# Kernel tuning notes

Measured on AMD Instinct MI355X. Metric: run time of the kernel, lower is better.

The kernel has to match this reference:

```python
import jax, jax.numpy as jnp
import numpy as np

SHAPES = [(64, 64), (32, 32), (16, 16), (8, 8)]  # (H, W) per level, sum HW = 5440
DIMS, NH, NLVL, NPTS, D_HEIGHT, NCAM, NQ, BS = 256, 8, 4, 8, 4, 6, 10000, 1


def ms_deform_attn(value, shapes, loc, attw):
    # value [B, sumHW, nH, dh]; loc [B, nq, nH, L, P, 2] in [0,1]; attw [B, nq, nH, L, P]
    B, _, nH, dh = value.shape
    nq, P = loc.shape[1], loc.shape[4]
    out = jnp.zeros((B, nH, nq, dh), value.dtype)
    start = 0
    for lvl, (h, w) in enumerate(shapes):
        v = value[:, start:start + h * w].transpose(0, 2, 1, 3)  # [B,nH,hw,dh]
        start += h * w
        l = loc[:, :, :, lvl].transpose(0, 2, 1, 3, 4)  # [B,nH,nq,P,2]
        x = l[..., 0] * w - 0.5
        y = l[..., 1] * h - 0.5
        x0, y0 = jnp.floor(x), jnp.floor(y)
        acc = jnp.zeros((B, nH, nq, P, dh), value.dtype)
        for dy in (0.0, 1.0):
            for dx in (0.0, 1.0):
                cx, cy = x0 + dx, y0 + dy
                wgt = (1.0 - jnp.abs(x - cx)) * (1.0 - jnp.abs(y - cy))
                valid = (cx >= 0) & (cx < w) & (cy >= 0) & (cy < h)
                xi = jnp.clip(cx, 0, w - 1).astype(jnp.int32)
                yi = jnp.clip(cy, 0, h - 1).astype(jnp.int32)
                idx = (yi * w + xi).reshape(B, nH, -1)  # [B,nH,nq*P]
                g = jnp.take_along_axis(v, idx[..., None], axis=2).reshape(B, nH, nq, P, dh)
                acc = acc + jnp.where(valid, wgt, 0.0)[..., None] * g
        aw = attw[:, :, :, lvl].transpose(0, 2, 1, 3)  # [B,nH,nq,P]
        out = out + jnp.einsum('bhqp,bhqpd->bhqd', aw, acc)
    return out.transpose(0, 2, 1, 3).reshape(B, nq, nH * dh)


def setup_inputs() -> dict:
    key = jax.random.key(0)
    ks = jax.random.split(key, 16)
    l = sum(h * w for h, w in SHAPES)
    s = 1.0 / np.sqrt(DIMS)
    inp = {
        'query': jax.random.normal(ks[0], (BS, NQ, DIMS), jnp.float32),
        'key': jax.random.normal(ks[1], (NCAM, l, BS, DIMS), jnp.float32),
        'value': jax.random.normal(ks[2], (NCAM, l, BS, DIMS), jnp.float32),
        'ref_points': jax.random.uniform(ks[3], (NCAM, BS, NQ, D_HEIGHT, 2), jnp.float32),
        'vox_mask': jax.random.randint(ks[4], (NCAM, BS, NQ, D_HEIGHT), 0, 2) > 0,
        'spatial_shapes': np.array(SHAPES, dtype=np.int64),
        'level_start_index': np.array([0, 4096, 5120, 5376], dtype=np.int64),
        'value_W': jax.random.uniform(ks[5], (DIMS, DIMS), jnp.float32, -s, s),
        'value_b': jnp.zeros((DIMS,), jnp.float32),
        'off_W': jax.random.normal(ks[6], (DIMS, NH * NLVL * NPTS * 2), jnp.float32) * 0.01,
        'off_b': jax.random.normal(ks[7], (NH * NLVL * NPTS * 2,), jnp.float32) * 0.1,
        'attw_W': jax.random.normal(ks[8], (DIMS, NH * NLVL * NPTS), jnp.float32) * 0.02,
        'attw_b': jnp.zeros((NH * NLVL * NPTS,), jnp.float32),
        'out_W': jax.random.uniform(ks[9], (DIMS, DIMS), jnp.float32, -s, s),
        'out_b': jnp.zeros((DIMS,), jnp.float32),
    }
    return inp


def reference(query, key, value, ref_points, vox_mask, spatial_shapes, level_start_index,
              value_W, value_b, off_W, off_b, attw_W, attw_b, out_W, out_b):
    shapes = [(int(h), int(w)) for h, w in np.asarray(spatial_shapes)]
    bs, nq, dims = query.shape
    cam = vox_mask.shape[0]
    B = bs * cam
    nH = NH
    dh = dims // nH
    Lv, P, D = len(shapes), NPTS, ref_points.shape[3]

    # value_proj; key unused by deformable attention math
    v = value.transpose(2, 0, 1, 3).reshape(B, -1, dims)
    v = (v @ value_W + value_b).reshape(B, -1, nH, dh)

    # rebatch: every camera sees the full (batch-0 visible) query set; padded
    # entries in the original are discarded, so computing all and masking is exact.
    q = jnp.broadcast_to(query[:, None], (bs, cam, nq, dims)).reshape(B, nq, dims)

    off = (q @ off_W + off_b).reshape(B, nq, nH, Lv, P, 2)
    attw = jax.nn.softmax((q @ attw_W + attw_b).reshape(B, nq, nH, Lv * P), -1)
    attw = attw.reshape(B, nq, nH, Lv, P)

    norm = jnp.array([[w, h] for h, w in shapes], q.dtype)  # [Lv,2] -> (W,H)
    off = off / norm[None, None, None, :, None, :]

    ref_rb = ref_points.transpose(1, 0, 2, 3, 4).reshape(B, nq, D, 2)
    off = off.reshape(B, nq, nH, Lv, P // D, D, 2)
    loc = (ref_rb[:, :, None, None, None] + off).reshape(B, nq, nH, Lv, P, 2)

    out = ms_deform_attn(v, shapes, loc, attw).reshape(bs, cam, nq, dims)

    valid = (vox_mask[:, 0].sum(-1) > 0).astype(q.dtype)  # [cam,nq] (batch-0 indexes, as original)
    slots = jnp.einsum('cq,bcqd->bqd', valid, out)
    count = (vox_mask.sum(-1) > 0).transpose(1, 2, 0).sum(-1).astype(q.dtype)
    count = jnp.maximum(count, 1.0)
    slots = slots / count[..., None]
    slots = slots @ out_W + out_b
    return slots + query  # dropout = identity (eval); inp_residual = query
```

## Files before the change

kernel.cpp:

```cpp
#include <hip/hip_runtime.h>


typedef unsigned short ushort_t;
typedef unsigned int uint_t;
typedef __attribute__((ext_vector_type(8))) short bf16x8;
typedef __attribute__((ext_vector_type(4))) float f32x4;
typedef __attribute__((ext_vector_type(2))) float f32x2;

__device__ __forceinline__ float bf2f(ushort_t u) {
    return __uint_as_float(((uint_t)u) << 16);
}
__device__ __forceinline__ ushort_t f2bf(float f) {
    uint_t i = __float_as_uint(f);
    uint_t r = i + 0x7fffu + ((i >> 16) & 1u);
    return (ushort_t)(r >> 16);
}
__device__ __forceinline__ bf16x8 pack8(float4 v0, float4 v1) {
    return (bf16x8){
        (short)f2bf(v0.x), (short)f2bf(v0.y), (short)f2bf(v0.z), (short)f2bf(v0.w),
        (short)f2bf(v1.x), (short)f2bf(v1.y), (short)f2bf(v1.z), (short)f2bf(v1.w)};
}

__global__ __launch_bounds__(256) void prep_w(
    const float* __restrict__ Wv, const float* __restrict__ Wo,
    const float* __restrict__ Wf, const float* __restrict__ Wa,
    ushort_t* __restrict__ Tv, ushort_t* __restrict__ To,
    ushort_t* __restrict__ Tqk) {
    const int z = blockIdx.z;
    const float* W;
    ushort_t* T;
    int N;
    if (z == 0)      { W = Wv; T = Tv;              N = 256; }
    else if (z == 1) { W = Wo; T = To;              N = 256; }
    else if (z == 2) { W = Wf; T = Tqk;             N = 512; }
    else             { W = Wa; T = Tqk + 512 * 256; N = 256; }
    const int n0 = blockIdx.y * 32;
    if (n0 >= N) return;
    const int k0 = blockIdx.x * 32;

    __shared__ float tile[32][33];
    const int tx = threadIdx.x & 31;
    const int ty = threadIdx.x >> 5;
    #pragma unroll
    for (int r = 0; r < 4; ++r) {
        const int k = ty + r * 8;
        tile[k][tx] = W[(size_t)(k0 + k) * N + n0 + tx];
    }
    __syncthreads();
    #pragma unroll
    for (int r = 0; r < 4; ++r) {
        const int n = ty + r * 8;
        T[(size_t)(n0 + n) * 256 + k0 + tx] = f2bf(tile[tx][n]);
    }
}

template <bool AF32, bool OUT_BF16, bool RESID>
__device__ __forceinline__ void gemm_body(
    ushort_t (*sA)[128][32], ushort_t (*sB)[128][32],
    const void* __restrict__ Av, const ushort_t* __restrict__ Wt,
    const float* __restrict__ bias0, const float* __restrict__ bias1, int split,
    const float* __restrict__ resid, void* __restrict__ Cv,
    int M, int N, int bx, int by) {
    const int m0 = bx * 128;
    const int n0 = by * 128;
    const int t    = threadIdx.x;
    const int lane = t & 63;
    const int w    = t >> 6;
    const int wr   = w >> 1, wc = w & 1;

    const int srow = t >> 2;
    const int skof = (t & 3) * 8;

    const bool am0 = (m0 + srow) < M;
    const bool am1 = (m0 + 64 + srow) < M;
    const float*    Af0 = (const float*)Av + (size_t)(m0 + srow) * 256 + skof;
    const float*    Af1 = Af0 + (size_t)64 * 256;
    const ushort_t* Ab0 = (const ushort_t*)Av + (size_t)(m0 + srow) * 256 + skof;
    const ushort_t* Ab1 = Ab0 + (size_t)64 * 256;
    const ushort_t* Bp0 = Wt + (size_t)(n0 + srow) * 256 + skof;
    const ushort_t* Bp1 = Bp0 + (size_t)64 * 256;

    const bf16x8 zz = {0, 0, 0, 0, 0, 0, 0, 0};

    auto loadA = [&](const float* af, const ushort_t* ab, int ko, bool ok) -> bf16x8 {
        if (!ok) return zz;
        if (AF32) {
            const float4 v0 = *(const float4*)(af + ko);
            const float4 v1 = *(const float4*)(af + ko + 4);
            return pack8(v0, v1);
        }
        return *(const bf16x8*)(ab + ko);
    };

    f32x4 acc[4][4];
    #pragma unroll
    for (int i = 0; i < 4; ++i)
        #pragma unroll
        for (int j = 0; j < 4; ++j)
            acc[i][j] = (f32x4){0.f, 0.f, 0.f, 0.f};

    {
        const bf16x8 a0 = loadA(Af0, Ab0, 0, am0);
        const bf16x8 a1 = loadA(Af1, Ab1, 0, am1);
        const bf16x8 b0 = *(const bf16x8*)(Bp0);
        const bf16x8 b1 = *(const bf16x8*)(Bp1);
        *(bf16x8*)(&sA[0][srow][skof])      = a0;
        *(bf16x8*)(&sA[0][64 + srow][skof]) = a1;
        *(bf16x8*)(&sB[0][srow][skof])      = b0;
        *(bf16x8*)(&sB[0][64 + srow][skof]) = b1;
    }
    __syncthreads();

    const int rl = lane & 15;
    const int kq = (lane >> 4) * 8;

    for (int k = 0; k < 8; ++k) {
        const int buf = k & 1;

        bf16x8 na0 = zz, na1 = zz, nb0 = zz, nb1 = zz;
        if (k < 7) {
            const int ko = (k + 1) * 32;
            na0 = loadA(Af0, Ab0, ko, am0);
            na1 = loadA(Af1, Ab1, ko, am1);
            nb0 = *(const bf16x8*)(Bp0 + ko);
            nb1 = *(const bf16x8*)(Bp1 + ko);
        }

        bf16x8 af[4], bfr[4];
        #pragma unroll
        for (int i = 0; i < 4; ++i)
            af[i] = *(const bf16x8*)(&sA[buf][wr * 64 + i * 16 + rl][kq]);
        #pragma unroll
        for (int j = 0; j < 4; ++j)
            bfr[j] = *(const bf16x8*)(&sB[buf][wc * 64 + j * 16 + rl][kq]);
        #pragma unroll
        for (int i = 0; i < 4; ++i)
            #pragma unroll
            for (int j = 0; j < 4; ++j)
                acc[i][j] = __builtin_amdgcn_mfma_f32_16x16x32_bf16(
                    af[i], bfr[j], acc[i][j], 0, 0, 0);

        if (k < 7) {
            __syncthreads();
            *(bf16x8*)(&sA[buf ^ 1][srow][skof])      = na0;
            *(bf16x8*)(&sA[buf ^ 1][64 + srow][skof]) = na1;
            *(bf16x8*)(&sB[buf ^ 1][srow][skof])      = nb0;
            *(bf16x8*)(&sB[buf ^ 1][64 + srow][skof]) = nb1;
            __syncthreads();
        }
    }

    const int col_l = lane & 15;
    const int rq    = (lane >> 4) * 4;
    #pragma unroll
    for (int j = 0; j < 4; ++j) {
        const int gn = n0 + wc * 64 + j * 16 + col_l;
        const float bj = (gn < split) ? bias0[gn] : bias1[gn - split];
        #pragma unroll
        for (int i = 0; i < 4; ++i) {
            #pragma unroll
            for (int r = 0; r < 4; ++r) {
                const int gm = m0 + wr * 64 + i * 16 + rq + r;
                if (gm >= M) continue;
                float v = acc[i][j][r] + bj;
                if (RESID) v += resid[(size_t)gm * N + gn];
                if (OUT_BF16)
                    ((ushort_t*)Cv)[(size_t)gm * N + gn] = f2bf(v);
                else
                    ((float*)Cv)[(size_t)gm * N + gn] = v;
            }
        }
    }
}

__global__ __launch_bounds__(256) void gemm_vqk(
    const float* __restrict__ value, const ushort_t* __restrict__ value_Wt,
    const float* __restrict__ value_b, ushort_t* __restrict__ vproj,
    const float* __restrict__ query, const ushort_t* __restrict__ qk_Wt,
    const float* __restrict__ off_b, const float* __restrict__ attw_b,
    float* __restrict__ qkcat) {
    __shared__ ushort_t sA[2][128][32];
    __shared__ ushort_t sB[2][128][32];
    int b = blockIdx.x;
    if (b < 510) {
        gemm_body<true, true, false>(sA, sB, value, value_Wt, value_b, value_b,
                                     256, nullptr, (void*)vproj, 32640, 256,
                                     b % 255, b / 255);
    } else {
        b -= 510;
        gemm_body<true, false, false>(sA, sB, query, qk_Wt, off_b, attw_b,
                                      512, nullptr, (void*)qkcat, 10000, 768,
                                      b % 79, b / 79);
    }
}

__global__ __launch_bounds__(256) void gemm_out_k(
    const ushort_t* __restrict__ slots, const ushort_t* __restrict__ out_Wt,
    const float* __restrict__ out_b, const float* __restrict__ query,
    float* __restrict__ out) {
    __shared__ ushort_t sA[2][128][32];
    __shared__ ushort_t sB[2][128][32];
    gemm_body<false, false, true>(sA, sB, slots, out_Wt, out_b, out_b, 256,
                                  query, (void*)out, 10000, 256,
                                  blockIdx.x, blockIdx.y);
}

__global__ __launch_bounds__(256) void sample_k(
    const float* __restrict__ qkcat,
    const float* __restrict__ refp,
    const int* __restrict__ vox,
    const ushort_t* __restrict__ vproj,
    ushort_t* __restrict__ slots) {
    const int q   = blockIdx.x;
    const int tid = threadIdx.x;
    const int lane  = tid & 63;
    const int h     = tid >> 5;
    const int lp    = tid & 31;
    const int slice = (tid >> 2) & 7;
    const int g     = tid & 3;

    __shared__ float s_valid[8];
    __shared__ float s_red[256][8];

    if (tid < 6) {
        const int base = (tid * 10000 + q) * 4;
        const int mm = vox[base] | vox[base + 1] | vox[base + 2] | vox[base + 3];
        s_valid[tid] = mm ? 1.0f : 0.0f;
    }

    const float a = qkcat[(size_t)q * 768 + 512 + tid];
    float mx = a;
    #pragma unroll
    for (int o = 16; o >= 1; o >>= 1) mx = fmaxf(mx, __shfl_xor(mx, o));
    const float e = __expf(a - mx);
    float se = e;
    #pragma unroll
    for (int o = 16; o >= 1; o >>= 1) se += __shfl_xor(se, o);
    const float aw = e / se;

    const int lvl = lp >> 3;
    const int p   = lp & 7;
    const int dd  = p & 3;
    const int   Sarr[4]   = {64, 32, 16, 8};
    const int   Lstart[4] = {0, 4096, 5120, 5376};
    const int   S  = Sarr[lvl];
    const float Sf = (float)S;
    const int   lstart = Lstart[lvl];
    const float ox = qkcat[(size_t)q * 768 + h * 64 + lvl * 16 + p * 2 + 0] / Sf;
    const float oy = qkcat[(size_t)q * 768 + h * 64 + lvl * 16 + p * 2 + 1] / Sf;

    __syncthreads();
    const float cnt = s_valid[0] + s_valid[1] + s_valid[2] +
                      s_valid[3] + s_valid[4] + s_valid[5];

    f32x2 acc2[4] = {{0.f, 0.f}, {0.f, 0.f}, {0.f, 0.f}, {0.f, 0.f}};
    const ushort_t* vp = vproj + (g << 3);
    const int srcbase = (lane & 32) + slice * 4;

    for (int c = 0; c < 6; ++c) {
        if (s_valid[c] == 0.0f) continue;

        int   ci0, ci1, ci2, ci3;
        float cw0, cw1, cw2, cw3;
        {
            const int rbase = ((c * 10000 + q) * 4 + dd) * 2;
            const float rx = refp[rbase + 0];
            const float ry = refp[rbase + 1];
            const float x  = (rx + ox) * Sf - 0.5f;
            const float y  = (ry + oy) * Sf - 0.5f;
            const float x0 = floorf(x), y0 = floorf(y);
            int   ci[4];
            float cw[4];
            #pragma unroll
            for (int k = 0; k < 4; ++k) {
                const float cx = x0 + (float)(k & 1);
                const float cy = y0 + (float)(k >> 1);
                const float wgt = (1.0f - fabsf(x - cx)) * (1.0f - fabsf(y - cy));
                const bool ok = (cx >= 0.0f) & (cx < Sf) & (cy >= 0.0f) & (cy < Sf);
                const int xi = (int)fminf(fmaxf(cx, 0.0f), Sf - 1.0f);
                const int yi = (int)fminf(fmaxf(cy, 0.0f), Sf - 1.0f);
                ci[k] = (c * 5440 + lstart + yi * S + xi) * 256 + h * 32;
                cw[k] = ok ? wgt * aw : 0.0f;
            }
            ci0 = ci[0]; ci1 = ci[1]; ci2 = ci[2]; ci3 = ci[3];
            cw0 = cw[0]; cw1 = cw[1]; cw2 = cw[2]; cw3 = cw[3];
        }

        #pragma unroll
        for (int j = 0; j < 4; ++j) {
            const int src = srcbase + j;
            const int i0 = __shfl(ci0, src), i1 = __shfl(ci1, src);
            const int i2 = __shfl(ci2, src), i3 = __shfl(ci3, src);
            const uint4 v0 = *(const uint4*)(vp + i0);
            const uint4 v1 = *(const uint4*)(vp + i1);
            const uint4 v2 = *(const uint4*)(vp + i2);
            const uint4 v3 = *(const uint4*)(vp + i3);
            const float w0 = __shfl(cw0, src), w1 = __shfl(cw1, src);
            const float w2 = __shfl(cw2, src), w3 = __shfl(cw3, src);
            const f32x2 W0 = {w0, w0}, W1 = {w1, w1}, W2 = {w2, w2}, W3 = {w3, w3};
            acc2[0] += W0 * (f32x2){__uint_as_float(v0.x << 16), __uint_as_float(v0.x & 0xffff0000u)};
            acc2[1] += W0 * (f32x2){__uint_as_float(v0.y << 16), __uint_as_float(v0.y & 0xffff0000u)};
            acc2[2] += W0 * (f32x2){__uint_as_float(v0.z << 16), __uint_as_float(v0.z & 0xffff0000u)};
            acc2[3] += W0 * (f32x2){__uint_as_float(v0.w << 16), __uint_as_float(v0.w & 0xffff0000u)};
            acc2[0] += W1 * (f32x2){__uint_as_float(v1.x << 16), __uint_as_float(v1.x & 0xffff0000u)};
            acc2[1] += W1 * (f32x2){__uint_as_float(v1.y << 16), __uint_as_float(v1.y & 0xffff0000u)};
            acc2[2] += W1 * (f32x2){__uint_as_float(v1.z << 16), __uint_as_float(v1.z & 0xffff0000u)};
            acc2[3] += W1 * (f32x2){__uint_as_float(v1.w << 16), __uint_as_float(v1.w & 0xffff0000u)};
            acc2[0] += W2 * (f32x2){__uint_as_float(v2.x << 16), __uint_as_float(v2.x & 0xffff0000u)};
            acc2[1] += W2 * (f32x2){__uint_as_float(v2.y << 16), __uint_as_float(v2.y & 0xffff0000u)};
            acc2[2] += W2 * (f32x2){__uint_as_float(v2.z << 16), __uint_as_float(v2.z & 0xffff0000u)};
            acc2[3] += W2 * (f32x2){__uint_as_float(v2.w << 16), __uint_as_float(v2.w & 0xffff0000u)};
            acc2[0] += W3 * (f32x2){__uint_as_float(v3.x << 16), __uint_as_float(v3.x & 0xffff0000u)};
            acc2[1] += W3 * (f32x2){__uint_as_float(v3.y << 16), __uint_as_float(v3.y & 0xffff0000u)};
            acc2[2] += W3 * (f32x2){__uint_as_float(v3.z << 16), __uint_as_float(v3.z & 0xffff0000u)};
            acc2[3] += W3 * (f32x2){__uint_as_float(v3.w << 16), __uint_as_float(v3.w & 0xffff0000u)};
        }
    }

    #pragma unroll
    for (int n = 0; n < 4; ++n) {
        s_red[tid][2 * n]     = acc2[n].x;
        s_red[tid][2 * n + 1] = acc2[n].y;
    }
    __syncthreads();

    const int cch = tid & 31;
    float sum = 0.0f;
    #pragma unroll
    for (int s = 0; s < 8; ++s)
        sum += s_red[h * 32 + s * 4 + (cch >> 3)][cch & 7];

    slots[(size_t)q * 256 + tid] = f2bf(sum / fmaxf(cnt, 1.0f));
}

extern "C" void kernel_launch(void* const* d_in, const int* in_sizes, int n_in,
                              void* d_out, int out_size, void* d_ws, size_t ws_size,
                              hipStream_t stream) {
    const float* query   = (const float*)d_in[0];
    const float* value   = (const float*)d_in[2];
    const float* refp    = (const float*)d_in[3];
    const int*   vox     = (const int*)d_in[4];
    const float* value_W = (const float*)d_in[7];
    const float* value_b = (const float*)d_in[8];
    const float* off_W   = (const float*)d_in[9];
    const float* off_b   = (const float*)d_in[10];
    const float* attw_W  = (const float*)d_in[11];
    const float* attw_b  = (const float*)d_in[12];
    const float* out_W   = (const float*)d_in[13];
    const float* out_b   = (const float*)d_in[14];
    float* out = (float*)d_out;

    char* ws = (char*)d_ws;
    ushort_t* vproj    = (ushort_t*)ws;
    float*    qkcat    = (float*)   (ws + 16711680);
    ushort_t* slots    = (ushort_t*)(ws + 47431680);
    ushort_t* value_Wt = (ushort_t*)(ws + 52551680);
    ushort_t* out_Wt   = (ushort_t*)(ws + 52551680 + 131072);
    ushort_t* qk_Wt    = (ushort_t*)(ws + 52551680 + 262144);

    prep_w<<<dim3(8, 16, 4), 256, 0, stream>>>(
        value_W, out_W, off_W, attw_W, value_Wt, out_Wt, qk_Wt);
    gemm_vqk<<<984, 256, 0, stream>>>(value, value_Wt, value_b, vproj,
                                      query, qk_Wt, off_b, attw_b, qkcat);
    sample_k<<<10000, 256, 0, stream>>>(qkcat, refp, vox, vproj, slots);
    gemm_out_k<<<dim3(79, 2), 256, 0, stream>>>(slots, out_Wt, out_b, query, out);
}
```

Baseline: 336.8 us.

## Store projected values in fp32, qk logits in bf16, reuse qkcat buffer for slots

Switches the value projection output to fp32 and the offset/attention-weight GEMM output to bf16, and writes the sampled slots back into the attention-logit region of the qkcat buffer, read with a 768 stride by the output GEMM. The bf16 packing is replaced with the hardware packed convert instruction via inline asm. The gather in the sampling kernel now loads twice the bytes per sampled value but avoids bf16 unpacking, while offsets and logits lose precision by going through bf16.

New measurement: 507.8 us. 50.8% more time.

```diff
diff --git a/kernel.cpp b/kernel.cpp
--- a/kernel.cpp
+++ b/kernel.cpp
@@ -16,9 +16,12 @@
     return (ushort_t)(r >> 16);
 }
 __device__ __forceinline__ bf16x8 pack8(float4 v0, float4 v1) {
-    return (bf16x8){
-        (short)f2bf(v0.x), (short)f2bf(v0.y), (short)f2bf(v0.z), (short)f2bf(v0.w),
-        (short)f2bf(v1.x), (short)f2bf(v1.y), (short)f2bf(v1.z), (short)f2bf(v1.w)};
+    union { uint_t u[4]; bf16x8 v; } r;
+    asm("v_cvt_pk_bf16_f32 %0, %1, %2" : "=v"(r.u[0]) : "v"(v0.x), "v"(v0.y));
+    asm("v_cvt_pk_bf16_f32 %0, %1, %2" : "=v"(r.u[1]) : "v"(v0.z), "v"(v0.w));
+    asm("v_cvt_pk_bf16_f32 %0, %1, %2" : "=v"(r.u[2]) : "v"(v1.x), "v"(v1.y));
+    asm("v_cvt_pk_bf16_f32 %0, %1, %2" : "=v"(r.u[3]) : "v"(v1.z), "v"(v1.w));
+    return r.v;
 }
 
 __global__ __launch_bounds__(256) void prep_w(
@@ -57,7 +60,7 @@
 template <bool AF32, bool OUT_BF16, bool RESID>
 __device__ __forceinline__ void gemm_body(
     ushort_t (*sA)[128][32], ushort_t (*sB)[128][32],
-    const void* __restrict__ Av, const ushort_t* __restrict__ Wt,
+    const void* __restrict__ Av, int Astride, const ushort_t* __restrict__ Wt,
     const float* __restrict__ bias0, const float* __restrict__ bias1, int split,
     const float* __restrict__ resid, void* __restrict__ Cv,
     int M, int N, int bx, int by) {
@@ -73,10 +76,10 @@
 
     const bool am0 = (m0 + srow) < M;
     const bool am1 = (m0 + 64 + srow) < M;
-    const float*    Af0 = (const float*)Av + (size_t)(m0 + srow) * 256 + skof;
-    const float*    Af1 = Af0 + (size_t)64 * 256;
-    const ushort_t* Ab0 = (const ushort_t*)Av + (size_t)(m0 + srow) * 256 + skof;
-    const ushort_t* Ab1 = Ab0 + (size_t)64 * 256;
+    const float*    Af0 = (const float*)Av + (size_t)(m0 + srow) * Astride + skof;
+    const float*    Af1 = Af0 + (size_t)64 * Astride;
+    const ushort_t* Ab0 = (const ushort_t*)Av + (size_t)(m0 + srow) * Astride + skof;
+    const ushort_t* Ab1 = Ab0 + (size_t)64 * Astride;
     const ushort_t* Bp0 = Wt + (size_t)(n0 + srow) * 256 + skof;
     const ushort_t* Bp1 = Bp0 + (size_t)64 * 256;
 
@@ -175,42 +178,42 @@
 
 __global__ __launch_bounds__(256) void gemm_vqk(
     const float* __restrict__ value, const ushort_t* __restrict__ value_Wt,
-    const float* __restrict__ value_b, ushort_t* __restrict__ vproj,
+    const float* __restrict__ value_b, float* __restrict__ vproj,
     const float* __restrict__ query, const ushort_t* __restrict__ qk_Wt,
     const float* __restrict__ off_b, const float* __restrict__ attw_b,
-    float* __restrict__ qkcat) {
+    ushort_t* __restrict__ qkcat) {
     __shared__ ushort_t sA[2][128][32];
     __shared__ ushort_t sB[2][128][32];
     int b = blockIdx.x;
     if (b < 510) {
-        gemm_body<true, true, false>(sA, sB, value, value_Wt, value_b, value_b,
-                                     256, nullptr, (void*)vproj, 32640, 256,
-                                     b % 255, b / 255);
+        gemm_body<true, false, false>(sA, sB, value, 256, value_Wt, value_b,
+                                      value_b, 256, nullptr, (void*)vproj,
+                                      32640, 256, b % 255, b / 255);
     } else {
         b -= 510;
-        gemm_body<true, false, false>(sA, sB, query, qk_Wt, off_b, attw_b,
-                                      512, nullptr, (void*)qkcat, 10000, 768,
-                                      b % 79, b / 79);
+        gemm_body<true, true, false>(sA, sB, query, 256, qk_Wt, off_b, attw_b,
+                                     512, nullptr, (void*)qkcat, 10000, 768,
+                                     b % 79, b / 79);
     }
 }
 
 __global__ __launch_bounds__(256) void gemm_out_k(
-    const ushort_t* __restrict__ slots, const ushort_t* __restrict__ out_Wt,
+    const ushort_t* __restrict__ slots,
+    const ushort_t* __restrict__ out_Wt,
     const float* __restrict__ out_b, const float* __restrict__ query,
     float* __restrict__ out) {
     __shared__ ushort_t sA[2][128][32];
     __shared__ ushort_t sB[2][128][32];
-    gemm_body<false, false, true>(sA, sB, slots, out_Wt, out_b, out_b, 256,
+    gemm_body<false, false, true>(sA, sB, slots, 768, out_Wt, out_b, out_b, 256,
                                   query, (void*)out, 10000, 256,
                                   blockIdx.x, blockIdx.y);
 }
 
 __global__ __launch_bounds__(256) void sample_k(
-    const float* __restrict__ qkcat,
+    ushort_t* __restrict__ qkcat,
     const float* __restrict__ refp,
     const int* __restrict__ vox,
-    const ushort_t* __restrict__ vproj,
-    ushort_t* __restrict__ slots) {
+    const float* __restrict__ vproj) {
     const int q   = blockIdx.x;
     const int tid = threadIdx.x;
     const int lane  = tid & 63;
@@ -228,7 +231,7 @@
         s_valid[tid] = mm ? 1.0f : 0.0f;
     }
 
-    const float a = qkcat[(size_t)q * 768 + 512 + tid];
+    const float a = bf2f(qkcat[(size_t)q * 768 + 512 + tid]);
     float mx = a;
     #pragma unroll
     for (int o = 16; o >= 1; o >>= 1) mx = fmaxf(mx, __shfl_xor(mx, o));
@@ -246,15 +249,15 @@
     const int   S  = Sarr[lvl];
     const float Sf = (float)S;
     const int   lstart = Lstart[lvl];
-    const float ox = qkcat[(size_t)q * 768 + h * 64 + lvl * 16 + p * 2 + 0] / Sf;
-    const float oy = qkcat[(size_t)q * 768 + h * 64 + lvl * 16 + p * 2 + 1] / Sf;
+    const float ox = bf2f(qkcat[(size_t)q * 768 + h * 64 + lvl * 16 + p * 2 + 0]) / Sf;
+    const float oy = bf2f(qkcat[(size_t)q * 768 + h * 64 + lvl * 16 + p * 2 + 1]) / Sf;
 
     __syncthreads();
     const float cnt = s_valid[0] + s_valid[1] + s_valid[2] +
                       s_valid[3] + s_valid[4] + s_valid[5];
 
     f32x2 acc2[4] = {{0.f, 0.f}, {0.f, 0.f}, {0.f, 0.f}, {0.f, 0.f}};
-    const ushort_t* vp = vproj + (g << 3);
+    const float* vp = vproj + (g << 3);
     const int srcbase = (lane & 32) + slice * 4;
 
     for (int c = 0; c < 6; ++c) {
@@ -291,29 +294,33 @@
             const int src = srcbase + j;
             const int i0 = __shfl(ci0, src), i1 = __shfl(ci1, src);
             const int i2 = __shfl(ci2, src), i3 = __shfl(ci3, src);
-            const uint4 v0 = *(const uint4*)(vp + i0);
-            const uint4 v1 = *(const uint4*)(vp + i1);
-            const uint4 v2 = *(const uint4*)(vp + i2);
-            const uint4 v3 = *(const uint4*)(vp + i3);
             const float w0 = __shfl(cw0, src), w1 = __shfl(cw1, src);
             const float w2 = __shfl(cw2, src), w3 = __shfl(cw3, src);
+            const f32x4 a0 = *(const f32x4*)(vp + i0);
+            const f32x4 b0 = *(const f32x4*)(vp + i0 + 4);
+            const f32x4 a1 = *(const f32x4*)(vp + i1);
+            const f32x4 b1 = *(const f32x4*)(vp + i1 + 4);
+            const f32x4 a2 = *(const f32x4*)(vp + i2);
+            const f32x4 b2 = *(const f32x4*)(vp + i2 + 4);
+            const f32x4 a3 = *(const f32x4*)(vp + i3);
+            const f32x4 b3 = *(const f32x4*)(vp + i3 + 4);
             const f32x2 W0 = {w0, w0}, W1 = {w1, w1}, W2 = {w2, w2}, W3 = {w3, w3};
-            acc2[0] += W0 * (f32x2){__uint_as_float(v0.x << 16), __uint_as_float(v0.x & 0xffff0000u)};
-            acc2[1] += W0 * (f32x2){__uint_as_float(v0.y << 16), __uint_as_float(v0.y & 0xffff0000u)};
-            acc2[2] += W0 * (f32x2){__uint_as_float(v0.z << 16), __uint_as_float(v0.z & 0xffff0000u)};
-            acc2[3] += W0 * (f32x2){__uint_as_float(v0.w << 16), __uint_as_float(v0.w & 0xffff0000u)};
-            acc2[0] += W1 * (f32x2){__uint_as_float(v1.x << 16), __uint_as_float(v1.x & 0xffff0000u)};
-            acc2[1] += W1 * (f32x2){__uint_as_float(v1.y << 16), __uint_as_float(v1.y & 0xffff0000u)};
-            acc2[2] += W1 * (f32x2){__uint_as_float(v1.z << 16), __uint_as_float(v1.z & 0xffff0000u)};
-            acc2[3] += W1 * (f32x2){__uint_as_float(v1.w << 16), __uint_as_float(v1.w & 0xffff0000u)};
-            acc2[0] += W2 * (f32x2){__uint_as_float(v2.x << 16), __uint_as_float(v2.x & 0xffff0000u)};
-            acc2[1] += W2 * (f32x2){__uint_as_float(v2.y << 16), __uint_as_float(v2.y & 0xffff0000u)};
-            acc2[2] += W2 * (f32x2){__uint_as_float(v2.z << 16), __uint_as_float(v2.z & 0xffff0000u)};
-            acc2[3] += W2 * (f32x2){__uint_as_float(v2.w << 16), __uint_as_float(v2.w & 0xffff0000u)};
-            acc2[0] += W3 * (f32x2){__uint_as_float(v3.x << 16), __uint_as_float(v3.x & 0xffff0000u)};
-            acc2[1] += W3 * (f32x2){__uint_as_float(v3.y << 16), __uint_as_float(v3.y & 0xffff0000u)};
-            acc2[2] += W3 * (f32x2){__uint_as_float(v3.z << 16), __uint_as_float(v3.z & 0xffff0000u)};
-            acc2[3] += W3 * (f32x2){__uint_as_float(v3.w << 16), __uint_as_float(v3.w & 0xffff0000u)};
+            acc2[0] += W0 * (f32x2){a0[0], a0[1]};
+            acc2[1] += W0 * (f32x2){a0[2], a0[3]};
+            acc2[2] += W0 * (f32x2){b0[0], b0[1]};
+            acc2[3] += W0 * (f32x2){b0[2], b0[3]};
+            acc2[0] += W1 * (f32x2){a1[0], a1[1]};
+            acc2[1] += W1 * (f32x2){a1[2], a1[3]};
+            acc2[2] += W1 * (f32x2){b1[0], b1[1]};
+            acc2[3] += W1 * (f32x2){b1[2], b1[3]};
+            acc2[0] += W2 * (f32x2){a2[0], a2[1]};
+            acc2[1] += W2 * (f32x2){a2[2], a2[3]};
+            acc2[2] += W2 * (f32x2){b2[0], b2[1]};
+            acc2[3] += W2 * (f32x2){b2[2], b2[3]};
+            acc2[0] += W3 * (f32x2){a3[0], a3[1]};
+            acc2[1] += W3 * (f32x2){a3[2], a3[3]};
+            acc2[2] += W3 * (f32x2){b3[0], b3[1]};
+            acc2[3] += W3 * (f32x2){b3[2], b3[3]};
         }
     }
 
@@ -330,7 +337,7 @@
     for (int s = 0; s < 8; ++s)
         sum += s_red[h * 32 + s * 4 + (cch >> 3)][cch & 7];
 
-    slots[(size_t)q * 256 + tid] = f2bf(sum / fmaxf(cnt, 1.0f));
+    qkcat[(size_t)q * 768 + 512 + tid] = f2bf(sum / fmaxf(cnt, 1.0f));
 }
 
 extern "C" void kernel_launch(void* const* d_in, const int* in_sizes, int n_in,
@@ -351,17 +358,17 @@
     float* out = (float*)d_out;
 
     char* ws = (char*)d_ws;
-    ushort_t* vproj    = (ushort_t*)ws;
-    float*    qkcat    = (float*)   (ws + 16711680);
-    ushort_t* slots    = (ushort_t*)(ws + 47431680);
-    ushort_t* value_Wt = (ushort_t*)(ws + 52551680);
-    ushort_t* out_Wt   = (ushort_t*)(ws + 52551680 + 131072);
-    ushort_t* qk_Wt    = (ushort_t*)(ws + 52551680 + 262144);
+    float*    vproj    = (float*)ws;
+    ushort_t* qkcat    = (ushort_t*)(ws + 33423360);
+    ushort_t* value_Wt = (ushort_t*)(ws + 48783360);
+    ushort_t* out_Wt   = (ushort_t*)(ws + 48783360 + 131072);
+    ushort_t* qk_Wt    = (ushort_t*)(ws + 48783360 + 262144);
 
     prep_w<<<dim3(8, 16, 4), 256, 0, stream>>>(
         value_W, out_W, off_W, attw_W, value_Wt, out_Wt, qk_Wt);
     gemm_vqk<<<984, 256, 0, stream>>>(value, value_Wt, value_b, vproj,
                                       query, qk_Wt, off_b, attw_b, qkcat);
-    sample_k<<<10000, 256, 0, stream>>>(qkcat, refp, vox, vproj, slots);
-    gemm_out_k<<<dim3(79, 2), 256, 0, stream>>>(slots, out_Wt, out_b, query, out);
-}
+    sample_k<<<10000, 256, 0, stream>>>(qkcat, refp, vox, vproj);
+    gemm_out_k<<<dim3(79, 2), 256, 0, stream>>>(qkcat + 512, out_Wt, out_b,
+                                                query, out);
+}
```
